# Kernel tuning notes

Hardware: AMD Instinct MI355X
Metric: run time of the kernel (lower is better)

The kernel has to match this reference:

```python
import jax, jax.numpy as jnp
import numpy as np

SS = 25.0 / 255.0   # spatial_scale = 1 / (SEARCH_SIZE/25), SEARCH_SIZE = 255
OUT = 7             # ROIPOOL_OUTSIZE // 4, ROIPOOL_OUTSIZE = 28
SP = 4              # sample_per_part (mmdet DeformRoIPooling default)
TRANS_STD = 0.1


def _deform_roi_pool(x, rois, offset):
    # x: [B,C,H,W]; rois: [N,5] (batch_idx,x1,y1,x2,y2); offset: [N,2,OUT,OUT] (ch0=x, ch1=y)
    B, C, H, W = x.shape
    N = rois.shape[0]
    b = rois[:, 0].astype(jnp.int32)
    sw = jnp.round(rois[:, 1]) * SS - 0.5
    sh = jnp.round(rois[:, 2]) * SS - 0.5
    rw = jnp.maximum((jnp.round(rois[:, 3]) + 1.0) * SS - 0.5 - sw, 0.1)
    rh = jnp.maximum((jnp.round(rois[:, 4]) + 1.0) * SS - 0.5 - sh, 0.1)
    bw, bh = rw / OUT, rh / OUT
    p = jnp.arange(OUT, dtype=x.dtype)
    tx = offset[:, 0] * TRANS_STD  # [N,OUT,OUT] indexed [n,ph,pw]
    ty = offset[:, 1] * TRANS_STD
    wstart = p[None, None, :] * bw[:, None, None] + sw[:, None, None] + tx * rw[:, None, None]
    hstart = p[None, :, None] * bh[:, None, None] + sh[:, None, None] + ty * rh[:, None, None]
    s = jnp.arange(SP, dtype=x.dtype)
    # sample coords [N,OUT,OUT,SP(ih),SP(iw)]
    sx = wstart[..., None, None] + s[None, None, None, None, :] * (bw / SP)[:, None, None, None, None]
    sy = hstart[..., None, None] + s[None, None, None, :, None] * (bh / SP)[:, None, None, None, None]
    valid = (sx >= -0.5) & (sx <= W - 0.5) & (sy >= -0.5) & (sy <= H - 0.5)
    xc = jnp.clip(sx, 0.0, W - 1.0)
    yc = jnp.clip(sy, 0.0, H - 1.0)
    x0 = jnp.floor(xc)
    y0 = jnp.floor(yc)
    dx = xc - x0
    dy = yc - y0
    xi0 = x0.astype(jnp.int32)
    yi0 = y0.astype(jnp.int32)
    xi1 = jnp.ceil(xc).astype(jnp.int32)
    yi1 = jnp.ceil(yc).astype(jnp.int32)
    feat = jnp.transpose(x, (0, 2, 3, 1))  # [B,H,W,C]
    bb = b[:, None, None, None, None]

    def g(yi, xi):
        return feat[bb, yi, xi]  # [N,OUT,OUT,SP,SP,C]

    val = (((1 - dx) * (1 - dy))[..., None] * g(yi0, xi0)
           + (dx * (1 - dy))[..., None] * g(yi0, xi1)
           + ((1 - dx) * dy)[..., None] * g(yi1, xi0)
           + (dx * dy)[..., None] * g(yi1, xi1))
    val = jnp.where(valid[..., None], val, 0.0)
    cnt = valid.sum(axis=(3, 4)).astype(x.dtype)              # [N,OUT,OUT]
    pooled = val.sum(axis=(3, 4)) / jnp.maximum(cnt, 1.0)[..., None]
    return jnp.transpose(pooled, (0, 3, 1, 2))                # [N,C,OUT,OUT]


def _lin(h, w, b):
    return h @ w.T + b


def _forward(x, rois, off_w1, off_b1, off_w2, off_b2, off_w3, off_b3,
             fc1_w, fc1_b, fc2_w, fc2_b, box_w, box_b):
    N = rois.shape[0]
    zero_off = jnp.zeros((N, 2, OUT, OUT), x.dtype)
    # pass 1: no-trans pooling -> offset prediction
    p0 = _deform_roi_pool(x, rois, zero_off).reshape(N, -1)
    h = jax.nn.relu(_lin(p0, off_w1, off_b1))
    h = jax.nn.relu(_lin(h, off_w2, off_b2))
    off = _lin(h, off_w3, off_b3).reshape(N, 2, OUT, OUT)
    # pass 2: deformable pooling with predicted offsets
    p = _deform_roi_pool(x, rois, off).reshape(N, -1)
    h = jax.nn.relu(_lin(p, fc1_w, fc1_b))
    h = jax.nn.relu(_lin(h, fc2_w, fc2_b))
    return _lin(h, box_w, box_b)  # [N,4]


def setup_inputs():
    key = jax.random.key(0)
    ks = jax.random.split(key, 16)
    B, C, H, W, N = 8, 256, 25, 25, 256
    IN = C * OUT * OUT  # 12544
    DFC, FCC = 1024, 512
    x = jax.random.normal(ks[0], (B, C, H, W), jnp.float32)
    bidx = jax.random.randint(ks[1], (N,), 0, B).astype(jnp.float32)
    x1 = jax.random.uniform(ks[2], (N,), minval=0.0, maxval=180.0)
    y1 = jax.random.uniform(ks[3], (N,), minval=0.0, maxval=180.0)
    wd = jax.random.uniform(ks[4], (N,), minval=24.0, maxval=120.0)
    ht = jax.random.uniform(ks[5], (N,), minval=24.0, maxval=120.0)
    rois = jnp.stack([bidx, x1, y1, jnp.clip(x1 + wd, 0.0, 254.0),
                      jnp.clip(y1 + ht, 0.0, 254.0)], axis=1)

    def lin_p(k, o, i):
        return jax.random.normal(k, (o, i), jnp.float32) * (1.0 / np.sqrt(i))

    return dict(
        x=x, rois=rois,
        off_w1=lin_p(ks[6], DFC, IN), off_b1=jnp.zeros((DFC,), jnp.float32),
        off_w2=lin_p(ks[7], DFC, DFC), off_b2=jnp.zeros((DFC,), jnp.float32),
        off_w3=lin_p(ks[8], 2 * OUT * OUT, DFC) * 0.1,
        off_b3=jnp.zeros((2 * OUT * OUT,), jnp.float32),
        fc1_w=lin_p(ks[9], FCC, IN), fc1_b=jnp.zeros((FCC,), jnp.float32),
        fc2_w=lin_p(ks[10], FCC, FCC), fc2_b=jnp.zeros((FCC,), jnp.float32),
        box_w=lin_p(ks[11], 4, FCC) * 0.001, box_b=jnp.zeros((4,), jnp.float32),
    )


def reference(x, rois, off_w1, off_b1, off_w2, off_b2, off_w3, off_b3,
              fc1_w, fc1_b, fc2_w, fc2_b, box_w, box_b):
    return _forward(x, rois, off_w1, off_b1, off_w2, off_b2, off_w3, off_b3,
                    fc1_w, fc1_b, fc2_w, fc2_b, box_w, box_b)
```

## Files before the change

### kernel.cpp

```cpp
#include <hip/hip_runtime.h>
#include <hip/hip_bf16.h>


#define NROI 256
#define NB   8
#define INF  12544
#define DFC  1024
#define FCC  512

typedef __attribute__((ext_vector_type(8))) short short8;
typedef __attribute__((ext_vector_type(4))) float floatx4;

static __device__ __forceinline__ unsigned short f2bf(float f) {
    unsigned int u = __float_as_uint(f);
    unsigned int r = (u + 0x7fffu + ((u >> 16) & 1u)) >> 16;
    return (unsigned short)r;
}

static __device__ __forceinline__ void async_copy16(const void* g, void* l) {
    __builtin_amdgcn_global_load_lds(
        (const __attribute__((address_space(1))) unsigned int*)g,
        (__attribute__((address_space(3))) unsigned int*)l, 16, 0, 0);
}

__global__ __launch_bounds__(256) void transpose_kernel(
        const float* __restrict__ x, float* __restrict__ xT) {
    __shared__ float t[32][33];
    int b  = blockIdx.z;
    int cb = blockIdx.y * 32;
    int lb = blockIdx.x * 32;
    int tx = threadIdx.x & 31, ty = threadIdx.x >> 5;
#pragma unroll
    for (int r = 0; r < 4; ++r) {
        int c = cb + ty + r * 8, l = lb + tx;
        if (l < 625) t[ty + r * 8][tx] = x[(size_t)(b * 256 + c) * 625 + l];
    }
    __syncthreads();
#pragma unroll
    for (int r = 0; r < 4; ++r) {
        int l = lb + ty + r * 8, c = cb + tx;
        if (l < 625) xT[((size_t)b * 625 + l) * 256 + c] = t[tx][ty + r * 8];
    }
}

__global__ __launch_bounds__(256) void pool_kernel(
        const float* __restrict__ feat, const float* __restrict__ rois,
        const float* __restrict__ off, int has_off,
        unsigned short* __restrict__ P) {
    __shared__ float sGrid[49][16];
    __shared__ int   sBase[49];
    __shared__ unsigned short sOut[128 * 49];
    const float SSC = (float)(25.0 / 255.0);
    int q = blockIdx.x;
    int n = blockIdx.y;
    int tid = threadIdx.x;

    if (tid < 49) {
        int bin = tid;
        const float* r = rois + n * 5;
        int b = (int)r[0];
        float sw = rintf(r[1]) * SSC - 0.5f;
        float sh = rintf(r[2]) * SSC - 0.5f;
        float rw = fmaxf((rintf(r[3]) + 1.0f) * SSC - 0.5f - sw, 0.1f);
        float rh = fmaxf((rintf(r[4]) + 1.0f) * SSC - 0.5f - sh, 0.1f);
        float bw = rw / 7.0f, bh = rh / 7.0f;
        float bws = bw * 0.25f, bhs = bh * 0.25f;
        int ph = bin / 7, pw = bin - ph * 7;
        float tx = 0.f, ty = 0.f;
        if (has_off) {
            tx = off[n * 98 + bin] * 0.1f;
            ty = off[n * 98 + 49 + bin] * 0.1f;
        }
        float wstart = pw * bw + sw + tx * rw;
        float hstart = ph * bh + sh + ty * rh;
#pragma unroll
        for (int i = 0; i < 16; ++i) sGrid[bin][i] = 0.f;
        int gy0 = 0, gx0 = 0, cnt = 0;
#pragma unroll
        for (int s = 0; s < 16; ++s) {
            float fx = wstart + (s & 3) * bws;
            float fy = hstart + (s >> 2) * bhs;
            bool valid = (fx >= -0.5f) && (fx <= 24.5f) && (fy >= -0.5f) && (fy <= 24.5f);
            float xc = fminf(fmaxf(fx, 0.f), 24.f);
            float yc = fminf(fmaxf(fy, 0.f), 24.f);
            float x0f = floorf(xc), y0f = floorf(yc);
            float dx = xc - x0f, dy = yc - y0f;
            int x0 = (int)x0f, y0 = (int)y0f;
            int x1 = (int)ceilf(xc), y1 = (int)ceilf(yc);
            if (s == 0) { gy0 = y0; gx0 = x0; }
            float w00 = (1.f - dx) * (1.f - dy), w01 = dx * (1.f - dy);
            float w10 = (1.f - dx) * dy,         w11 = dx * dy;
            if (!valid) { w00 = w01 = w10 = w11 = 0.f; }
            cnt += valid ? 1 : 0;
            int ry0 = (y0 - gy0) * 4, ry1 = (y1 - gy0) * 4;
            sGrid[bin][ry0 + (x0 - gx0)] += w00;
            sGrid[bin][ry0 + (x1 - gx0)] += w01;
            sGrid[bin][ry1 + (x0 - gx0)] += w10;
            sGrid[bin][ry1 + (x1 - gx0)] += w11;
        }
        float inv = 1.0f / fmaxf((float)cnt, 1.0f);
#pragma unroll
        for (int i = 0; i < 16; ++i) sGrid[bin][i] *= inv;
        sBase[bin] = gy0 | (gx0 << 8) | (b << 16);
    }
    __syncthreads();

    int wv = tid >> 6, lane = tid & 63;
    int cbase = q * 128 + lane * 2;
    for (int bin = wv; bin < 49; bin += 4) {
        int base = sBase[bin];
        int gy0 = base & 255, gx0 = (base >> 8) & 255, b = base >> 16;
        const float4* wp = (const float4*)sGrid[bin];
        float4 w0 = wp[0], w1 = wp[1], w2 = wp[2], w3 = wp[3];
        float ww[16] = { w0.x, w0.y, w0.z, w0.w, w1.x, w1.y, w1.z, w1.w,
                         w2.x, w2.y, w2.z, w2.w, w3.x, w3.y, w3.z, w3.w };
        int rowOff[4], colOff[4];
#pragma unroll
        for (int r = 0; r < 4; ++r) {
            rowOff[r] = min(gy0 + r, 24) * 25;
            colOff[r] = min(gx0 + r, 24);
        }
        int b625 = b * 625;
        float ax = 0.f, ay = 0.f;
#pragma unroll
        for (int cell = 0; cell < 16; ++cell) {
            int pix = b625 + rowOff[cell >> 2] + colOff[cell & 3];
            float2 v = *(const float2*)(feat + (size_t)pix * 256 + cbase);
            ax += ww[cell] * v.x;
            ay += ww[cell] * v.y;
        }
        sOut[(lane * 2) * 49 + bin] = f2bf(ax);
        sOut[(lane * 2 + 1) * 49 + bin] = f2bf(ay);
    }
    __syncthreads();
    const uint2* so = (const uint2*)sOut;
    uint2* dp = (uint2*)(P + (size_t)n * INF + q * 128 * 49);
    for (int i = tid; i < 128 * 49 / 4; i += 256) dp[i] = so[i];
}

__global__ __launch_bounds__(256) void gemm_pipe(
        const unsigned short* __restrict__ A, const float* __restrict__ Bw,
        float* __restrict__ Cpart, int N, int K, int kSteps) {
    constexpr int BM = 256, BN = 64;
    constexpr int FM = 4, FN = 4;
    __shared__ unsigned short As[2][BM * 32];
    __shared__ float          Bs[2][BN * 32];
    const int tid = threadIdx.x;
    const int lane = tid & 63;
    const int wave = tid >> 6;
    const int n0 = blockIdx.x * BN;
    const int k0 = blockIdx.z * kSteps * 32;
    const int quad = lane >> 4;
    const int l16 = lane & 15;

    floatx4 acc[FM][FN];
#pragma unroll
    for (int i = 0; i < FM; ++i)
#pragma unroll
        for (int j = 0; j < FN; ++j) acc[i][j] = (floatx4)0.f;

    const unsigned short* ag[4];
    int albase[4];
#pragma unroll
    for (int i = 0; i < 4; ++i) {
        int idx = tid + i * 256;
        int row = idx >> 2;
        int kg4 = (idx & 3) ^ ((row >> 1) & 3);
        ag[i] = A + (size_t)row * K + kg4 * 8;
        albase[i] = (i * 256 + wave * 64) * 16;
    }
    const float* bg[2];
    int blbase[2];
#pragma unroll
    for (int i = 0; i < 2; ++i) {
        int idx = tid + i * 256;
        int row = idx >> 3;
        int kg = (idx & 7) ^ ((row >> 1) & 7);
        bg[i] = Bw + (size_t)(n0 + row) * K + kg * 4;
        blbase[i] = (i * 256 + wave * 64) * 16;
    }

    auto issue = [&](int slot, int kk) {
#pragma unroll
        for (int i = 0; i < 4; ++i)
            async_copy16(ag[i] + kk, (char*)&As[slot][0] + albase[i]);
#pragma unroll
        for (int i = 0; i < 2; ++i)
            async_copy16(bg[i] + kk, (char*)&Bs[slot][0] + blbase[i]);
    };

    issue(0, k0);
    __syncthreads();

    int cur = 0;
    for (int ks = 0; ks < kSteps; ++ks) {
        if (ks + 1 < kSteps) issue(cur ^ 1, k0 + (ks + 1) * 32);
        short8 a[FM], bf[FN];
#pragma unroll
        for (int i = 0; i < FM; ++i) {
            int r = wave * 64 + i * 16 + l16;
            int sl = quad ^ ((r >> 1) & 3);
            a[i] = *(const short8*)(&As[cur][0] + r * 32 + sl * 8);
        }
#pragma unroll
        for (int j = 0; j < FN; ++j) {
            int r = j * 16 + l16;
            int sw8 = (r >> 1) & 7;
            int g0 = (quad * 2) ^ sw8;
            int g1 = (quad * 2 + 1) ^ sw8;
            float4 v0 = *(const float4*)(&Bs[cur][0] + r * 32 + g0 * 4);
            float4 v1 = *(const float4*)(&Bs[cur][0] + r * 32 + g1 * 4);
            bf[j][0] = (short)f2bf(v0.x); bf[j][1] = (short)f2bf(v0.y);
            bf[j][2] = (short)f2bf(v0.z); bf[j][3] = (short)f2bf(v0.w);
            bf[j][4] = (short)f2bf(v1.x); bf[j][5] = (short)f2bf(v1.y);
            bf[j][6] = (short)f2bf(v1.z); bf[j][7] = (short)f2bf(v1.w);
        }
#pragma unroll
        for (int i = 0; i < FM; ++i)
#pragma unroll
            for (int j = 0; j < FN; ++j)
                acc[i][j] = __builtin_amdgcn_mfma_f32_16x16x32_bf16(a[i], bf[j], acc[i][j], 0, 0, 0);
        __syncthreads();
        cur ^= 1;
    }
    float* Cp = Cpart + (size_t)blockIdx.z * BM * N;
#pragma unroll
    for (int i = 0; i < FM; ++i)
#pragma unroll
        for (int rr = 0; rr < 4; ++rr) {
            int row = wave * 64 + i * 16 + quad * 4 + rr;
            float* cr = Cp + (size_t)row * N + n0;
#pragma unroll
            for (int j = 0; j < FN; ++j)
                cr[j * 16 + l16] = acc[i][j][rr];
        }
}

__global__ __launch_bounds__(256) void reduce_bias(
        const float* __restrict__ part, int zc, int mn4,
        const float* __restrict__ bias, int nmask, int relu,
        unsigned short* __restrict__ obf, float* __restrict__ of) {
    int idx = blockIdx.x * 256 + threadIdx.x;
    if (idx >= mn4) return;
    int idx4 = idx * 4;
    const float* bp = bias + (idx4 & nmask);
    float4 acc = *(const float4*)bp;
    const float4* p = (const float4*)part + idx;
    for (int z = 0; z < zc; ++z) {
        float4 v = p[(size_t)z * mn4];
        acc.x += v.x; acc.y += v.y; acc.z += v.z; acc.w += v.w;
    }
    if (relu) {
        acc.x = fmaxf(acc.x, 0.f); acc.y = fmaxf(acc.y, 0.f);
        acc.z = fmaxf(acc.z, 0.f); acc.w = fmaxf(acc.w, 0.f);
    }
    if (obf) {
        ushort4 h;
        h.x = f2bf(acc.x); h.y = f2bf(acc.y); h.z = f2bf(acc.z); h.w = f2bf(acc.w);
        *(ushort4*)(obf + idx4) = h;
    }
    if (of) *(float4*)(of + idx4) = acc;
}

__global__ __launch_bounds__(256) void fc_small(
        const float* __restrict__ h2, const float* __restrict__ w3,
        const float* __restrict__ b3, float* __restrict__ out) {
    __shared__ float shl[2][1024];
    int n2 = blockIdx.x * 2;
    int tid = threadIdx.x;
    for (int i = tid; i < 2048; i += 256)
        shl[i >> 10][i & 1023] = fmaxf(h2[(size_t)n2 * 1024 + i], 0.f);
    __syncthreads();
    int h = tid >> 7, o = tid & 127;
    if (o < 98) {
        float acc = b3[o];
        const float* w = w3 + (size_t)o * 1024;
        const float* s = shl[h];
        for (int k = 0; k < 1024; k += 4) {
            float4 wv = *(const float4*)(w + k);
            acc += s[k] * wv.x + s[k + 1] * wv.y + s[k + 2] * wv.z + s[k + 3] * wv.w;
        }
        out[(n2 + h) * 98 + o] = acc;
    }
}

__global__ __launch_bounds__(64) void head_kernel(
        const float* __restrict__ h4, const float* __restrict__ bw,
        const float* __restrict__ bb, float* __restrict__ out) {
    int n = blockIdx.x, t = threadIdx.x;
    float a0 = 0, a1 = 0, a2 = 0, a3 = 0;
    for (int k = t; k < 512; k += 64) {
        float v = fmaxf(h4[(size_t)n * 512 + k], 0.f);
        a0 += v * bw[k]; a1 += v * bw[512 + k];
        a2 += v * bw[1024 + k]; a3 += v * bw[1536 + k];
    }
#pragma unroll
    for (int o = 32; o > 0; o >>= 1) {
        a0 += __shfl_down(a0, o); a1 += __shfl_down(a1, o);
        a2 += __shfl_down(a2, o); a3 += __shfl_down(a3, o);
    }
    if (t == 0) {
        out[n * 4 + 0] = a0 + bb[0]; out[n * 4 + 1] = a1 + bb[1];
        out[n * 4 + 2] = a2 + bb[2]; out[n * 4 + 3] = a3 + bb[3];
    }
}

extern "C" void kernel_launch(void* const* d_in, const int* in_sizes, int n_in,
                              void* d_out, int out_size, void* d_ws, size_t ws_size,
                              hipStream_t stream) {
    const float* x      = (const float*)d_in[0];
    const float* rois   = (const float*)d_in[1];
    const float* off_w1 = (const float*)d_in[2];
    const float* off_b1 = (const float*)d_in[3];
    const float* off_w2 = (const float*)d_in[4];
    const float* off_b2 = (const float*)d_in[5];
    const float* off_w3 = (const float*)d_in[6];
    const float* off_b3 = (const float*)d_in[7];
    const float* fc1_w  = (const float*)d_in[8];
    const float* fc1_b  = (const float*)d_in[9];
    const float* fc2_w  = (const float*)d_in[10];
    const float* fc2_b  = (const float*)d_in[11];
    const float* box_w  = (const float*)d_in[12];
    const float* box_b  = (const float*)d_in[13];
    float* out = (float*)d_out;

    char* ws = (char*)d_ws;
    size_t o = 0;
    auto carve = [&](size_t bytes) { char* p = ws + o; o += (bytes + 255) & ~(size_t)255; return p; };
    float*          xT   = (float*)carve((size_t)NB * 625 * 256 * 4);
    unsigned short* P    = (unsigned short*)carve((size_t)NROI * INF * 2);
    unsigned short* h1b  = (unsigned short*)carve((size_t)NROI * DFC * 2);
    float*          h2   = (float*)carve((size_t)NROI * DFC * 4);
    float*          offb = (float*)carve((size_t)NROI * 98 * 4);
    unsigned short* h3b  = (unsigned short*)carve((size_t)NROI * FCC * 2);
    float*          h4   = (float*)carve((size_t)NROI * FCC * 4);
    size_t fixed = o;
    const size_t SLAB = (size_t)NROI * DFC * 4;
    int zg1;
    if      (ws_size >= fixed + 28 * SLAB) zg1 = 28;
    else if (ws_size >= fixed + 14 * SLAB) zg1 = 14;
    else                                   zg1 = 7;
    int zg4 = zg1 * 2;
    float* part = (float*)carve((size_t)zg1 * SLAB);

    transpose_kernel<<<dim3(20, 8, 8), 256, 0, stream>>>(x, xT);
    pool_kernel<<<dim3(2, NROI), 256, 0, stream>>>(xT, rois, nullptr, 0, P);
    gemm_pipe<<<dim3(16, 1, zg1), 256, 0, stream>>>(P, off_w1, part, DFC, INF, 392 / zg1);
    reduce_bias<<<256, 256, 0, stream>>>(part, zg1, NROI * DFC / 4, off_b1, DFC - 1, 1, h1b, nullptr);
    gemm_pipe<<<dim3(16, 1, 8), 256, 0, stream>>>(h1b, off_w2, part, DFC, DFC, 4);
    reduce_bias<<<256, 256, 0, stream>>>(part, 8, NROI * DFC / 4, off_b2, DFC - 1, 0, nullptr, h2);
    fc_small<<<128, 256, 0, stream>>>(h2, off_w3, off_b3, offb);
    pool_kernel<<<dim3(2, NROI), 256, 0, stream>>>(xT, rois, offb, 1, P);
    gemm_pipe<<<dim3(8, 1, zg4), 256, 0, stream>>>(P, fc1_w, part, FCC, INF, 392 / zg4);
    reduce_bias<<<128, 256, 0, stream>>>(part, zg4, NROI * FCC / 4, fc1_b, FCC - 1, 1, h3b, nullptr);
    gemm_pipe<<<dim3(8, 1, 8), 256, 0, stream>>>(h3b, fc2_w, part, FCC, FCC, 2);
    reduce_bias<<<128, 256, 0, stream>>>(part, 8, NROI * FCC / 4, fc2_b, FCC - 1, 0, nullptr, h4);
    head_kernel<<<NROI, 64, 0, stream>>>(h4, box_w, box_b, out);
}
```

Measured before the change: 291.1 us.

## Convert B weights to bf16 once at staging and fuse split-K reductions into consumers

The GEMM now loads each fp32 weight tile through registers, converts it to bf16 once, and stores it into a half-size LDS buffer. Previously the async copy kept fp32 in LDS and every wave reconverted it per fragment. The fp32 global loads are issued before the MFMA block so they overlap compute, at the cost of extra VGPRs and no longer using async global-to-LDS copies for B. Separately, the split-K reduction plus bias for the second and fourth GEMMs is folded into fc_small and the head kernel, removing two launches and the h2/h4 round trips.

```diff
diff --git a/kernel.cpp b/kernel.cpp
--- a/kernel.cpp
+++ b/kernel.cpp
@@ -144,7 +144,7 @@
     constexpr int BM = 256, BN = 64;
     constexpr int FM = 4, FN = 4;
     __shared__ unsigned short As[2][BM * 32];
-    __shared__ float          Bs[2][BN * 32];
+    __shared__ unsigned short Bs[2][BN * 32];
     const int tid = threadIdx.x;
     const int lane = tid & 63;
     const int wave = tid >> 6;
@@ -169,32 +169,44 @@
         ag[i] = A + (size_t)row * K + kg4 * 8;
         albase[i] = (i * 256 + wave * 64) * 16;
     }
-    const float* bg[2];
-    int blbase[2];
-#pragma unroll
-    for (int i = 0; i < 2; ++i) {
-        int idx = tid + i * 256;
-        int row = idx >> 3;
-        int kg = (idx & 7) ^ ((row >> 1) & 7);
-        bg[i] = Bw + (size_t)(n0 + row) * K + kg * 4;
-        blbase[i] = (i * 256 + wave * 64) * 16;
-    }
-
-    auto issue = [&](int slot, int kk) {
+    const int brow = tid >> 2;
+    const int bkg  = (tid & 3) ^ ((brow >> 1) & 3);
+    const float* bgp = Bw + (size_t)(n0 + brow) * K + bkg * 8;
+    unsigned short* const bl0 = &Bs[0][tid * 8];
+    unsigned short* const bl1 = &Bs[1][tid * 8];
+
+    auto issueA = [&](int slot, int kk) {
 #pragma unroll
         for (int i = 0; i < 4; ++i)
             async_copy16(ag[i] + kk, (char*)&As[slot][0] + albase[i]);
-#pragma unroll
-        for (int i = 0; i < 2; ++i)
-            async_copy16(bg[i] + kk, (char*)&Bs[slot][0] + blbase[i]);
     };
-
-    issue(0, k0);
+    auto packB = [&](float4 v0, float4 v1) {
+        short8 w;
+        w[0] = (short)f2bf(v0.x); w[1] = (short)f2bf(v0.y);
+        w[2] = (short)f2bf(v0.z); w[3] = (short)f2bf(v0.w);
+        w[4] = (short)f2bf(v1.x); w[5] = (short)f2bf(v1.y);
+        w[6] = (short)f2bf(v1.z); w[7] = (short)f2bf(v1.w);
+        return w;
+    };
+
+    issueA(0, k0);
+    {
+        float4 v0 = *(const float4*)(bgp + k0);
+        float4 v1 = *(const float4*)(bgp + k0 + 4);
+        *(short8*)bl0 = packB(v0, v1);
+    }
     __syncthreads();
 
     int cur = 0;
     for (int ks = 0; ks < kSteps; ++ks) {
-        if (ks + 1 < kSteps) issue(cur ^ 1, k0 + (ks + 1) * 32);
+        const bool hn = (ks + 1 < kSteps);
+        const int kn = k0 + (ks + 1) * 32;
+        float4 v0, v1;
+        if (hn) {
+            issueA(cur ^ 1, kn);
+            v0 = *(const float4*)(bgp + kn);
+            v1 = *(const float4*)(bgp + kn + 4);
+        }
         short8 a[FM], bf[FN];
 #pragma unroll
         for (int i = 0; i < FM; ++i) {
@@ -205,21 +217,15 @@
 #pragma unroll
         for (int j = 0; j < FN; ++j) {
             int r = j * 16 + l16;
-            int sw8 = (r >> 1) & 7;
-            int g0 = (quad * 2) ^ sw8;
-            int g1 = (quad * 2 + 1) ^ sw8;
-            float4 v0 = *(const float4*)(&Bs[cur][0] + r * 32 + g0 * 4);
-            float4 v1 = *(const float4*)(&Bs[cur][0] + r * 32 + g1 * 4);
-            bf[j][0] = (short)f2bf(v0.x); bf[j][1] = (short)f2bf(v0.y);
-            bf[j][2] = (short)f2bf(v0.z); bf[j][3] = (short)f2bf(v0.w);
-            bf[j][4] = (short)f2bf(v1.x); bf[j][5] = (short)f2bf(v1.y);
-            bf[j][6] = (short)f2bf(v1.z); bf[j][7] = (short)f2bf(v1.w);
+            int sl = quad ^ ((r >> 1) & 3);
+            bf[j] = *(const short8*)(&Bs[cur][0] + r * 32 + sl * 8);
         }
 #pragma unroll
         for (int i = 0; i < FM; ++i)
 #pragma unroll
             for (int j = 0; j < FN; ++j)
                 acc[i][j] = __builtin_amdgcn_mfma_f32_16x16x32_bf16(a[i], bf[j], acc[i][j], 0, 0, 0);
+        if (hn) *(short8*)(cur ? bl0 : bl1) = packB(v0, v1);
         __syncthreads();
         cur ^= 1;
     }
@@ -262,14 +268,20 @@
     if (of) *(float4*)(of + idx4) = acc;
 }
 
-__global__ __launch_bounds__(256) void fc_small(
-        const float* __restrict__ h2, const float* __restrict__ w3,
+__global__ __launch_bounds__(256) void fc_small_red(
+        const float* __restrict__ part, int zc,
+        const float* __restrict__ b2, const float* __restrict__ w3,
         const float* __restrict__ b3, float* __restrict__ out) {
     __shared__ float shl[2][1024];
     int n2 = blockIdx.x * 2;
     int tid = threadIdx.x;
-    for (int i = tid; i < 2048; i += 256)
-        shl[i >> 10][i & 1023] = fmaxf(h2[(size_t)n2 * 1024 + i], 0.f);
+    for (int i = tid; i < 2048; i += 256) {
+        int n = n2 + (i >> 10), k = i & 1023;
+        float acc = b2[k];
+        for (int z = 0; z < zc; ++z)
+            acc += part[(size_t)z * (NROI * DFC) + n * 1024 + k];
+        shl[i >> 10][k] = fmaxf(acc, 0.f);
+    }
     __syncthreads();
     int h = tid >> 7, o = tid & 127;
     if (o < 98) {
@@ -284,13 +296,17 @@
     }
 }
 
-__global__ __launch_bounds__(64) void head_kernel(
-        const float* __restrict__ h4, const float* __restrict__ bw,
+__global__ __launch_bounds__(64) void head_red(
+        const float* __restrict__ part, int zc,
+        const float* __restrict__ b4, const float* __restrict__ bw,
         const float* __restrict__ bb, float* __restrict__ out) {
     int n = blockIdx.x, t = threadIdx.x;
     float a0 = 0, a1 = 0, a2 = 0, a3 = 0;
     for (int k = t; k < 512; k += 64) {
-        float v = fmaxf(h4[(size_t)n * 512 + k], 0.f);
+        float acc = b4[k];
+        for (int z = 0; z < zc; ++z)
+            acc += part[(size_t)z * (NROI * FCC) + n * 512 + k];
+        float v = fmaxf(acc, 0.f);
         a0 += v * bw[k]; a1 += v * bw[512 + k];
         a2 += v * bw[1024 + k]; a3 += v * bw[1536 + k];
     }
@@ -330,10 +346,8 @@
     float*          xT   = (float*)carve((size_t)NB * 625 * 256 * 4);
     unsigned short* P    = (unsigned short*)carve((size_t)NROI * INF * 2);
     unsigned short* h1b  = (unsigned short*)carve((size_t)NROI * DFC * 2);
-    float*          h2   = (float*)carve((size_t)NROI * DFC * 4);
     float*          offb = (float*)carve((size_t)NROI * 98 * 4);
     unsigned short* h3b  = (unsigned short*)carve((size_t)NROI * FCC * 2);
-    float*          h4   = (float*)carve((size_t)NROI * FCC * 4);
     size_t fixed = o;
     const size_t SLAB = (size_t)NROI * DFC * 4;
     int zg1;
@@ -348,12 +362,10 @@
     gemm_pipe<<<dim3(16, 1, zg1), 256, 0, stream>>>(P, off_w1, part, DFC, INF, 392 / zg1);
     reduce_bias<<<256, 256, 0, stream>>>(part, zg1, NROI * DFC / 4, off_b1, DFC - 1, 1, h1b, nullptr);
     gemm_pipe<<<dim3(16, 1, 8), 256, 0, stream>>>(h1b, off_w2, part, DFC, DFC, 4);
-    reduce_bias<<<256, 256, 0, stream>>>(part, 8, NROI * DFC / 4, off_b2, DFC - 1, 0, nullptr, h2);
-    fc_small<<<128, 256, 0, stream>>>(h2, off_w3, off_b3, offb);
+    fc_small_red<<<128, 256, 0, stream>>>(part, 8, off_b2, off_w3, off_b3, offb);
     pool_kernel<<<dim3(2, NROI), 256, 0, stream>>>(xT, rois, offb, 1, P);
     gemm_pipe<<<dim3(8, 1, zg4), 256, 0, stream>>>(P, fc1_w, part, FCC, INF, 392 / zg4);
     reduce_bias<<<128, 256, 0, stream>>>(part, zg4, NROI * FCC / 4, fc1_b, FCC - 1, 1, h3b, nullptr);
     gemm_pipe<<<dim3(8, 1, 8), 256, 0, stream>>>(h3b, fc2_w, part, FCC, FCC, 2);
-    reduce_bias<<<128, 256, 0, stream>>>(part, 8, NROI * FCC / 4, fc2_b, FCC - 1, 0, nullptr, h4);
-    head_kernel<<<NROI, 64, 0, stream>>>(h4, box_w, box_b, out);
-}
+    head_red<<<NROI, 64, 0, stream>>>(part, 8, fc2_b, box_w, box_b, out);
+}
```

Result: slower. 309.9 us (+6.5%).
